# Kernel optimization log

Measured on AMD Instinct MI355X. Metric: run time of the kernel, lower is better.

The kernel has to match this reference:

```python
import jax, jax.numpy as jnp
import numpy as np

N = 50000
E = 800000


def gcn_conv(x, W, b, src, dst, n_nodes):
    # PyG GCNConv: add self-loops, symmetric deg^-1/2 normalization,
    # out[dst] += norm * (x @ W)[src], then bias.
    h = x @ W  # [N, out]
    src_sl = jnp.concatenate([src, jnp.arange(n_nodes, dtype=src.dtype)])
    dst_sl = jnp.concatenate([dst, jnp.arange(n_nodes, dtype=dst.dtype)])
    deg = jax.ops.segment_sum(jnp.ones_like(dst_sl, dtype=h.dtype), dst_sl,
                              num_segments=n_nodes)  # in-degree incl. self-loop
    dinv = jnp.where(deg > 0, jax.lax.rsqrt(deg), 0.0)
    norm = dinv[src_sl] * dinv[dst_sl]  # [E+N]
    msg = norm[:, None] * h[src_sl]  # gather + scale, [E+N, out]
    out = jax.ops.segment_sum(msg, dst_sl, num_segments=n_nodes)
    return out + b


def setup_inputs() -> dict:
    key = jax.random.key(0)
    ks = jax.random.split(key, 8)
    F, H, O = 128, 128, 64
    x = jax.random.normal(ks[0], (N, F), dtype=jnp.float32)
    edge_index = jax.random.randint(ks[1], (2, E), 0, N, dtype=jnp.int64)
    # Glorot-ish scaled weights
    W1 = jax.random.normal(ks[2], (F, H), dtype=jnp.float32) / np.sqrt(F)
    b1 = jnp.zeros((H,), dtype=jnp.float32)
    W2 = jax.random.normal(ks[3], (H, H), dtype=jnp.float32) / np.sqrt(H)
    b2 = jnp.zeros((H,), dtype=jnp.float32)
    W3 = jax.random.normal(ks[4], (H, O), dtype=jnp.float32) / np.sqrt(H)
    b3 = jnp.zeros((O,), dtype=jnp.float32)
    return {"x": x, "edge_index": edge_index, "W1": W1, "b1": b1,
            "W2": W2, "b2": b2, "W3": W3, "b3": b3}


def reference(x, edge_index, W1, b1, W2, b2, W3, b3):
    src, dst = edge_index[0], edge_index[1]
    h = gcn_conv(x, W1, b1, src, dst, N)
    h = jax.nn.elu(h)
    h = gcn_conv(h, W2, b2, src, dst, N)
    h = jax.nn.elu(h)
    h = gcn_conv(h, W3, b3, src, dst, N)
    return h
```

## Files before the change

### kernel.cpp

```cpp
#include <hip/hip_runtime.h>
#include <hip/hip_fp16.h>
#include <math.h>


#define NFEAT_IN 128
#define SCAN_CHUNK 2048

typedef _Float16 f16x8 __attribute__((ext_vector_type(8)));
typedef float f32x4 __attribute__((ext_vector_type(4)));

__global__ void zero_kernel(int4* __restrict__ p, int n4, int4* __restrict__ eswpad) {
    int i = blockIdx.x * blockDim.x + threadIdx.x;
    int4 z; z.x = z.y = z.z = z.w = 0;
    if (i < n4) p[i] = z;
    if (i < 8) eswpad[i] = z;
}

__global__ __launch_bounds__(256) void countrank_kernel(const int* __restrict__ dst,
                                                        int* __restrict__ cnt,
                                                        int* __restrict__ rank, int E) {
    int i = blockIdx.x * blockDim.x + threadIdx.x;
    int base = i * 4;
    if (base + 4 <= E) {
        int4 d = *(const int4*)&dst[base];
        int4 r;
        r.x = atomicAdd(&cnt[d.x], 1);
        r.y = atomicAdd(&cnt[d.y], 1);
        r.z = atomicAdd(&cnt[d.z], 1);
        r.w = atomicAdd(&cnt[d.w], 1);
        *(int4*)&rank[base] = r;
    } else {
        for (int k = base; k < E; ++k) rank[k] = atomicAdd(&cnt[dst[k]], 1);
    }
}

__global__ __launch_bounds__(256) void reduce_kernel(const int* __restrict__ cnt,
                                                     int* __restrict__ bsum, int n) {
    __shared__ int wtot[4];
    int b = blockIdx.x, t = threadIdx.x;
    int base = b * SCAN_CHUNK + t * 8;
    int s = 0;
    if (base + 8 <= n) {
        int4 a = *(const int4*)&cnt[base];
        int4 c = *(const int4*)&cnt[base + 4];
        s = a.x + a.y + a.z + a.w + c.x + c.y + c.z + c.w;
    } else {
        for (int i = 0; i < 8; ++i) if (base + i < n) s += cnt[base + i];
    }
    int lane = t & 63, wid = t >> 6;
    #pragma unroll
    for (int off = 32; off > 0; off >>= 1) s += __shfl_down(s, off, 64);
    if (lane == 0) wtot[wid] = s;
    __syncthreads();
    if (t == 0) bsum[b] = wtot[0] + wtot[1] + wtot[2] + wtot[3];
}

__global__ __launch_bounds__(256) void scan3_kernel(const int* __restrict__ cnt,
                                                    const int* __restrict__ bsum,
                                                    int* __restrict__ offs,
                                                    float* __restrict__ dinv,
                                                    int n, int nb) {
    __shared__ int wtot[4];
    __shared__ int sbase;
    int b = blockIdx.x, t = threadIdx.x;
    if (t < 64) {
        int val = (t < nb) ? bsum[t] : 0;
        int pre = (t < b) ? val : 0;
        int tot = val;
        #pragma unroll
        for (int off = 32; off > 0; off >>= 1) {
            pre += __shfl_down(pre, off, 64);
            tot += __shfl_down(tot, off, 64);
        }
        if (t == 0) {
            sbase = pre;
            if (b == nb - 1) offs[n] = tot;
        }
    }
    int base = b * SCAN_CHUNK + t * 8;
    int v[8];
    #pragma unroll
    for (int i = 0; i < 8; ++i) v[i] = (base + i < n) ? cnt[base + i] : 0;
    int psum[8], s = 0;
    #pragma unroll
    for (int i = 0; i < 8; ++i) { psum[i] = s; s += v[i]; }
    int lane = t & 63, wid = t >> 6;
    int inc = s;
    #pragma unroll
    for (int off = 1; off < 64; off <<= 1) {
        int tt = __shfl_up(inc, off, 64);
        if (lane >= off) inc += tt;
    }
    if (lane == 63) wtot[wid] = inc;
    __syncthreads();
    int wb = 0;
    for (int w = 0; w < wid; ++w) wb += wtot[w];
    int tbase = sbase + wb + (inc - s);
    #pragma unroll
    for (int i = 0; i < 8; ++i) {
        if (base + i < n) {
            offs[base + i] = tbase + psum[i];
            dinv[base + i] = rsqrtf((float)(v[i] + 1));
        }
    }
}

__global__ __launch_bounds__(256) void fillr_kernel(const int* __restrict__ src,
                                                    const int* __restrict__ dst,
                                                    const int* __restrict__ rank,
                                                    const int* __restrict__ offs,
                                                    const float* __restrict__ dinv,
                                                    int2* __restrict__ esw, int E) {
    int i = blockIdx.x * blockDim.x + threadIdx.x;
    int base = i * 4;
    if (base + 4 <= E) {
        int4 d = *(const int4*)&dst[base];
        int4 r = *(const int4*)&rank[base];
        int4 s = *(const int4*)&src[base];
        int p0 = offs[d.x] + r.x;
        int p1 = offs[d.y] + r.y;
        int p2 = offs[d.z] + r.z;
        int p3 = offs[d.w] + r.w;
        float w0 = dinv[s.x], w1 = dinv[s.y], w2 = dinv[s.z], w3 = dinv[s.w];
        __half2 h0 = __floats2half2_rn(w0, w0);
        __half2 h1 = __floats2half2_rn(w1, w1);
        __half2 h2 = __floats2half2_rn(w2, w2);
        __half2 h3 = __floats2half2_rn(w3, w3);
        int2 e0; e0.x = s.x; e0.y = *(int*)&h0;
        int2 e1; e1.x = s.y; e1.y = *(int*)&h1;
        int2 e2; e2.x = s.z; e2.y = *(int*)&h2;
        int2 e3; e3.x = s.w; e3.y = *(int*)&h3;
        esw[p0] = e0; esw[p1] = e1; esw[p2] = e2; esw[p3] = e3;
    } else {
        for (int k = base; k < E; ++k) {
            int d = dst[k];
            int p = offs[d] + rank[k];
            int s = src[k];
            float w = dinv[s];
            __half2 h = __floats2half2_rn(w, w);
            int2 e; e.x = s; e.y = *(int*)&h;
            esw[p] = e;
        }
    }
}

__global__ __launch_bounds__(256) void convx_kernel(const float* __restrict__ x,
                                                    f16x8* __restrict__ Xf, int nchunk) {
    int i = blockIdx.x * blockDim.x + threadIdx.x;
    if (i >= nchunk) return;
    int m = i >> 4, kc = i & 15;
    float4 a = *(const float4*)&x[(size_t)m * 128 + kc * 8];
    float4 b = *(const float4*)&x[(size_t)m * 128 + kc * 8 + 4];
    f16x8 v;
    v[0] = (_Float16)a.x; v[1] = (_Float16)a.y; v[2] = (_Float16)a.z; v[3] = (_Float16)a.w;
    v[4] = (_Float16)b.x; v[5] = (_Float16)b.y; v[6] = (_Float16)b.z; v[7] = (_Float16)b.w;
    int kt = kc >> 2, sub = kc & 3;
    Xf[(size_t)((m >> 4) * 4 + kt) * 64 + sub * 16 + (m & 15)] = v;
}

__global__ void wfrag_kernel(const float* __restrict__ W1, const float* __restrict__ W2,
                             const float* __restrict__ W3, f16x8* __restrict__ wf1,
                             f16x8* __restrict__ wf2, f16x8* __restrict__ wf3) {
    int b = blockIdx.x;
    const float* W; f16x8* Wf; int NT;
    if (b < 8)       { W = W1; Wf = wf1; NT = 8; }
    else if (b < 16) { W = W2; Wf = wf2; NT = 8; b -= 8; }
    else             { W = W3; Wf = wf3; NT = 4; b -= 16; }
    int c = b * 256 + threadIdx.x;
    if (c >= NT * 256) return;
    int BN = NT * 16;
    int nt = c >> 8;
    int kt = (c >> 6) & 3;
    int l = c & 63;
    int n = nt * 16 + (l & 15);
    int k0 = kt * 32 + (l >> 4) * 8;
    f16x8 v;
    #pragma unroll
    for (int j = 0; j < 8; ++j) v[j] = (_Float16)W[(size_t)(k0 + j) * BN + n];
    Wf[c] = v;
}

template <int NT>
__global__ __launch_bounds__(256) void mgemm_kernel(const f16x8* __restrict__ Xf,
                                                    const f16x8* __restrict__ Wg,
                                                    __half* __restrict__ Y, int mtiles) {
    constexpr int BN = NT * 16;
    __shared__ f16x8 Wf[NT * 4 * 64];
    int t = threadIdx.x;
    #pragma unroll
    for (int i = 0; i < NT; ++i) Wf[t + i * 256] = Wg[t + i * 256];
    __syncthreads();
    int lane = t & 63;
    int mt0 = blockIdx.x * 8 + (t >> 6) * 2;
    #pragma unroll
    for (int it = 0; it < 2; ++it) {
        int mtile = mt0 + it;
        if (mtile >= mtiles) continue;
        const f16x8* xb = Xf + (size_t)mtile * 4 * 64;
        f16x8 bf[4];
        #pragma unroll
        for (int kt = 0; kt < 4; ++kt) bf[kt] = xb[kt * 64 + lane];
        f32x4 acc[NT];
        #pragma unroll
        for (int nt = 0; nt < NT; ++nt) acc[nt] = (f32x4){0.f, 0.f, 0.f, 0.f};
        #pragma unroll
        for (int kt = 0; kt < 4; ++kt) {
            #pragma unroll
            for (int nt = 0; nt < NT; ++nt) {
                f16x8 af = Wf[(nt * 4 + kt) * 64 + lane];
                acc[nt] = __builtin_amdgcn_mfma_f32_16x16x32_f16(af, bf[kt], acc[nt], 0, 0, 0);
            }
        }
        int m = mtile * 16 + (lane & 15);
        int nc0 = (lane >> 4) * 4;
        #pragma unroll
        for (int nt = 0; nt < NT; ++nt) {
            union { __half2 h2[2]; uint2 u; } pk;
            pk.h2[0] = __floats2half2_rn(acc[nt][0], acc[nt][1]);
            pk.h2[1] = __floats2half2_rn(acc[nt][2], acc[nt][3]);
            *(uint2*)&Y[(size_t)m * BN + nt * 16 + nc0] = pk.u;
        }
    }
}

__global__ __launch_bounds__(256) void agg128_kernel(const __half* __restrict__ H,
                                                     const int* __restrict__ offs,
                                                     const int2* __restrict__ esw,
                                                     const float* __restrict__ dinv,
                                                     const float* __restrict__ bias,
                                                     uint4* __restrict__ outf, int n) {
    int lane = threadIdx.x & 63;
    int q = lane >> 4;
    int fl = lane & 15;
    int v = blockIdx.x * 4 + (threadIdx.x >> 6);
    if (v >= n) return;
    float dv = dinv[v];
    int e0 = offs[v], e1 = offs[v + 1];
    int cntE = e1 - e0;
    int nfull = cntE >> 4;
    const char* Hb = (const char*)H + fl * 16;
    __half2 acc[4];
    __half2 zh = __floats2half2_rn(0.f, 0.f);
    acc[0] = zh; acc[1] = zh; acc[2] = zh; acc[3] = zh;
    int e = e0 + q;
    for (int i = 0; i < nfull; ++i, e += 16) {
        #pragma unroll
        for (int j = 0; j < 4; ++j) {
            int2 p = esw[e + 4 * j];
            __half2 w2 = *(__half2*)&p.y;
            uint4 hq = *(const uint4*)(Hb + ((size_t)(unsigned)p.x << 8));
            const __half2* h2 = (const __half2*)&hq;
            acc[0] = __hfma2(h2[0], w2, acc[0]);
            acc[1] = __hfma2(h2[1], w2, acc[1]);
            acc[2] = __hfma2(h2[2], w2, acc[2]);
            acc[3] = __hfma2(h2[3], w2, acc[3]);
        }
    }
    if (cntE & 15) {
        #pragma unroll
        for (int j = 0; j < 4; ++j) {
            int ee = e + 4 * j;
            int2 p = esw[ee];
            int wi = (ee < e1) ? p.y : 0;
            __half2 w2 = *(__half2*)&wi;
            uint4 hq = *(const uint4*)(Hb + ((size_t)(unsigned)p.x << 8));
            const __half2* h2 = (const __half2*)&hq;
            acc[0] = __hfma2(h2[0], w2, acc[0]);
            acc[1] = __hfma2(h2[1], w2, acc[1]);
            acc[2] = __hfma2(h2[2], w2, acc[2]);
            acc[3] = __hfma2(h2[3], w2, acc[3]);
        }
    }
    #pragma unroll
    for (int m = 16; m <= 32; m <<= 1) {
        #pragma unroll
        for (int k = 0; k < 4; ++k) {
            int ai = *(int*)&acc[k];
            int bi = __shfl_xor(ai, m, 64);
            acc[k] = __hadd2(acc[k], *(__half2*)&bi);
        }
    }
    if (q == 0) {
        float a[8];
        #pragma unroll
        for (int k = 0; k < 4; ++k) {
            float2 f = __half22float2(acc[k]);
            a[2 * k] = f.x; a[2 * k + 1] = f.y;
        }
        uint4 hq = *(const uint4*)(Hb + ((size_t)(unsigned)v << 8));
        const _Float16* hp = (const _Float16*)&hq;
        float b[8];
        *(float4*)&b[0] = *(const float4*)&bias[fl * 8];
        *(float4*)&b[4] = *(const float4*)&bias[fl * 8 + 4];
        float r[8];
        #pragma unroll
        for (int k = 0; k < 8; ++k) {
            float t2 = fmaf((float)hp[k], dv, a[k]);
            r[k] = fmaf(dv, t2, b[k]);
            r[k] = r[k] > 0.f ? r[k] : (__expf(r[k]) - 1.f);
        }
        union { __half2 h2[4]; uint4 u; } pk;
        pk.h2[0] = __floats2half2_rn(r[0], r[1]);
        pk.h2[1] = __floats2half2_rn(r[2], r[3]);
        pk.h2[2] = __floats2half2_rn(r[4], r[5]);
        pk.h2[3] = __floats2half2_rn(r[6], r[7]);
        int blockc = (v >> 4) * 4 + (fl >> 2);
        int l2 = (fl & 3) * 16 + (v & 15);
        outf[(size_t)blockc * 64 + l2] = pk.u;
    }
}

__global__ __launch_bounds__(256) void agg64_kernel(const __half* __restrict__ H,
                                                    const int* __restrict__ offs,
                                                    const int2* __restrict__ esw,
                                                    const float* __restrict__ dinv,
                                                    const float* __restrict__ bias,
                                                    float* __restrict__ out, int n) {
    int lane = threadIdx.x & 63;
    int q = lane >> 3;
    int fl = lane & 7;
    int v = blockIdx.x * 4 + (threadIdx.x >> 6);
    if (v >= n) return;
    float dv = dinv[v];
    int e0 = offs[v], e1 = offs[v + 1];
    int cntE = e1 - e0;
    int nfull = cntE >> 4;
    const char* Hb = (const char*)H + fl * 16;
    __half2 acc[4];
    __half2 zh = __floats2half2_rn(0.f, 0.f);
    acc[0] = zh; acc[1] = zh; acc[2] = zh; acc[3] = zh;
    int e = e0 + q;
    for (int i = 0; i < nfull; ++i, e += 16) {
        #pragma unroll
        for (int j = 0; j < 2; ++j) {
            int2 p = esw[e + 8 * j];
            __half2 w2 = *(__half2*)&p.y;
            uint4 hq = *(const uint4*)(Hb + ((size_t)(unsigned)p.x << 7));
            const __half2* h2 = (const __half2*)&hq;
            acc[0] = __hfma2(h2[0], w2, acc[0]);
            acc[1] = __hfma2(h2[1], w2, acc[1]);
            acc[2] = __hfma2(h2[2], w2, acc[2]);
            acc[3] = __hfma2(h2[3], w2, acc[3]);
        }
    }
    if (cntE & 15) {
        #pragma unroll
        for (int j = 0; j < 2; ++j) {
            int ee = e + 8 * j;
            int2 p = esw[ee];
            int wi = (ee < e1) ? p.y : 0;
            __half2 w2 = *(__half2*)&wi;
            uint4 hq = *(const uint4*)(Hb + ((size_t)(unsigned)p.x << 7));
            const __half2* h2 = (const __half2*)&hq;
            acc[0] = __hfma2(h2[0], w2, acc[0]);
            acc[1] = __hfma2(h2[1], w2, acc[1]);
            acc[2] = __hfma2(h2[2], w2, acc[2]);
            acc[3] = __hfma2(h2[3], w2, acc[3]);
        }
    }
    #pragma unroll
    for (int m = 8; m <= 32; m <<= 1) {
        #pragma unroll
        for (int k = 0; k < 4; ++k) {
            int ai = *(int*)&acc[k];
            int bi = __shfl_xor(ai, m, 64);
            acc[k] = __hadd2(acc[k], *(__half2*)&bi);
        }
    }
    if (q == 0) {
        float a[8];
        #pragma unroll
        for (int k = 0; k < 4; ++k) {
            float2 f = __half22float2(acc[k]);
            a[2 * k] = f.x; a[2 * k + 1] = f.y;
        }
        uint4 hq = *(const uint4*)(Hb + ((size_t)(unsigned)v << 7));
        const _Float16* hp = (const _Float16*)&hq;
        float b[8];
        *(float4*)&b[0] = *(const float4*)&bias[fl * 8];
        *(float4*)&b[4] = *(const float4*)&bias[fl * 8 + 4];
        float r[8];
        #pragma unroll
        for (int k = 0; k < 8; ++k) {
            float t2 = fmaf((float)hp[k], dv, a[k]);
            r[k] = fmaf(dv, t2, b[k]);
        }
        float4 o0, o1;
        o0.x = r[0]; o0.y = r[1]; o0.z = r[2]; o0.w = r[3];
        o1.x = r[4]; o1.y = r[5]; o1.z = r[6]; o1.w = r[7];
        *(float4*)&out[(size_t)v * 64 + fl * 8] = o0;
        *(float4*)&out[(size_t)v * 64 + fl * 8 + 4] = o1;
    }
}

static inline size_t alignup(size_t x) { return (x + 255) & ~(size_t)255; }

extern "C" void kernel_launch(void* const* d_in, const int* in_sizes, int n_in,
                              void* d_out, int out_size, void* d_ws, size_t ws_size,
                              hipStream_t stream) {
    const float* x  = (const float*)d_in[0];
    const int*   ei = (const int*)d_in[1];
    const float* W1 = (const float*)d_in[2];
    const float* b1 = (const float*)d_in[3];
    const float* W2 = (const float*)d_in[4];
    const float* b2 = (const float*)d_in[5];
    const float* W3 = (const float*)d_in[6];
    const float* b3 = (const float*)d_in[7];
    float* out = (float*)d_out;

    const int N = in_sizes[0] / NFEAT_IN;
    const int E = in_sizes[1] / 2;
    const int* src = ei;
    const int* dst = ei + E;

    char* w = (char*)d_ws;
    int* cnt  = (int*)w;  w += alignup((size_t)N * sizeof(int));
    int* rank = (int*)w;  w += alignup((size_t)E * sizeof(int));
    int* offs = (int*)w;  w += alignup((size_t)(N + 1) * sizeof(int));
    float* dinv = (float*)w; w += alignup((size_t)N * sizeof(float));
    int* bsum = (int*)w;  w += alignup((size_t)64 * sizeof(int));
    int2* esw = (int2*)w; w += alignup((size_t)(E + 16) * sizeof(int2));
    __half* fA = (__half*)w; w += alignup((size_t)N * 128 * sizeof(__half));
    __half* hB = (__half*)w; w += alignup((size_t)N * 128 * sizeof(__half));
    f16x8* wf1 = (f16x8*)w; w += alignup((size_t)2048 * sizeof(f16x8));
    f16x8* wf2 = (f16x8*)w; w += alignup((size_t)2048 * sizeof(f16x8));
    f16x8* wf3 = (f16x8*)w; w += alignup((size_t)1024 * sizeof(f16x8));

    const int nb = (N + SCAN_CHUNK - 1) / SCAN_CHUNK;
    const int mtiles = N / 16;
    const int egrid = (E / 4 + 255) / 256;

    zero_kernel<<<(N / 4 + 255) / 256, 256, 0, stream>>>((int4*)cnt, N / 4, (int4*)(esw + E));
    countrank_kernel<<<egrid, 256, 0, stream>>>(dst, cnt, rank, E);
    reduce_kernel<<<nb, 256, 0, stream>>>(cnt, bsum, N);
    scan3_kernel<<<nb, 256, 0, stream>>>(cnt, bsum, offs, dinv, N, nb);
    fillr_kernel<<<egrid, 256, 0, stream>>>(src, dst, rank, offs, dinv, esw, E);

    wfrag_kernel<<<20, 256, 0, stream>>>(W1, W2, W3, wf1, wf2, wf3);
    convx_kernel<<<(N * 16 + 255) / 256, 256, 0, stream>>>(x, (f16x8*)fA, N * 16);

    int gemm_grid = (mtiles + 7) / 8;
    int agg_grid = (N + 3) / 4;

    mgemm_kernel<8><<<gemm_grid, 256, 0, stream>>>((const f16x8*)fA, wf1, hB, mtiles);
    agg128_kernel<<<agg_grid, 256, 0, stream>>>(hB, offs, esw, dinv, b1, (uint4*)fA, N);
    mgemm_kernel<8><<<gemm_grid, 256, 0, stream>>>((const f16x8*)fA, wf2, hB, mtiles);
    agg128_kernel<<<agg_grid, 256, 0, stream>>>(hB, offs, esw, dinv, b2, (uint4*)fA, N);
    mgemm_kernel<4><<<gemm_grid, 256, 0, stream>>>((const f16x8*)fA, wf3, hB, mtiles);
    agg64_kernel<<<agg_grid, 256, 0, stream>>>(hB, offs, esw, dinv, b3, out, N);
}
```

Baseline: 193.4 us.

## Split 128-wide hidden features into two 64-column planes for aggregation

The GEMM now writes its 128-column fp16 output as two separate N×64 planes. The 128-wide aggregation runs twice as many blocks, each handling one half of the features for a node with 8 lanes per edge row. This shrinks the gathered working set per pass to 128-byte rows, aiming to improve L2/cache hit rates for the random src gathers. The cost is that edge indices and weights are read twice and twice as many blocks are launched.

```diff
diff --git a/kernel.cpp b/kernel.cpp
--- a/kernel.cpp
+++ b/kernel.cpp
@@ -183,8 +183,8 @@
 template <int NT>
 __global__ __launch_bounds__(256) void mgemm_kernel(const f16x8* __restrict__ Xf,
                                                     const f16x8* __restrict__ Wg,
-                                                    __half* __restrict__ Y, int mtiles) {
-    constexpr int BN = NT * 16;
+                                                    __half* __restrict__ Y, int mtiles,
+                                                    size_t hstride) {
     __shared__ f16x8 Wf[NT * 4 * 64];
     int t = threadIdx.x;
     #pragma unroll
@@ -218,37 +218,38 @@
             union { __half2 h2[2]; uint2 u; } pk;
             pk.h2[0] = __floats2half2_rn(acc[nt][0], acc[nt][1]);
             pk.h2[1] = __floats2half2_rn(acc[nt][2], acc[nt][3]);
-            *(uint2*)&Y[(size_t)m * BN + nt * 16 + nc0] = pk.u;
-        }
-    }
-}
-
-__global__ __launch_bounds__(256) void agg128_kernel(const __half* __restrict__ H,
-                                                     const int* __restrict__ offs,
-                                                     const int2* __restrict__ esw,
-                                                     const float* __restrict__ dinv,
-                                                     const float* __restrict__ bias,
-                                                     uint4* __restrict__ outf, int n) {
+            *(uint2*)&Y[(size_t)(nt >> 2) * hstride + (size_t)m * 64 + (nt & 3) * 16 + nc0] = pk.u;
+        }
+    }
+}
+
+__global__ __launch_bounds__(256) void agg128h_kernel(const __half* __restrict__ H,
+                                                      const int* __restrict__ offs,
+                                                      const int2* __restrict__ esw,
+                                                      const float* __restrict__ dinv,
+                                                      const float* __restrict__ bias,
+                                                      uint4* __restrict__ outf, int n) {
+    int half = blockIdx.x & 1;
     int lane = threadIdx.x & 63;
-    int q = lane >> 4;
-    int fl = lane & 15;
-    int v = blockIdx.x * 4 + (threadIdx.x >> 6);
+    int q = lane >> 3;
+    int fl = lane & 7;
+    int v = (blockIdx.x >> 1) * 4 + (threadIdx.x >> 6);
     if (v >= n) return;
     float dv = dinv[v];
     int e0 = offs[v], e1 = offs[v + 1];
     int cntE = e1 - e0;
     int nfull = cntE >> 4;
-    const char* Hb = (const char*)H + fl * 16;
+    const char* Hb = (const char*)H + (size_t)half * n * 128 + fl * 16;
     __half2 acc[4];
     __half2 zh = __floats2half2_rn(0.f, 0.f);
     acc[0] = zh; acc[1] = zh; acc[2] = zh; acc[3] = zh;
     int e = e0 + q;
     for (int i = 0; i < nfull; ++i, e += 16) {
         #pragma unroll
-        for (int j = 0; j < 4; ++j) {
-            int2 p = esw[e + 4 * j];
+        for (int j = 0; j < 2; ++j) {
+            int2 p = esw[e + 8 * j];
             __half2 w2 = *(__half2*)&p.y;
-            uint4 hq = *(const uint4*)(Hb + ((size_t)(unsigned)p.x << 8));
+            uint4 hq = *(const uint4*)(Hb + ((size_t)(unsigned)p.x << 7));
             const __half2* h2 = (const __half2*)&hq;
             acc[0] = __hfma2(h2[0], w2, acc[0]);
             acc[1] = __hfma2(h2[1], w2, acc[1]);
@@ -258,12 +259,12 @@
     }
     if (cntE & 15) {
         #pragma unroll
-        for (int j = 0; j < 4; ++j) {
-            int ee = e + 4 * j;
+        for (int j = 0; j < 2; ++j) {
+            int ee = e + 8 * j;
             int2 p = esw[ee];
             int wi = (ee < e1) ? p.y : 0;
             __half2 w2 = *(__half2*)&wi;
-            uint4 hq = *(const uint4*)(Hb + ((size_t)(unsigned)p.x << 8));
+            uint4 hq = *(const uint4*)(Hb + ((size_t)(unsigned)p.x << 7));
             const __half2* h2 = (const __half2*)&hq;
             acc[0] = __hfma2(h2[0], w2, acc[0]);
             acc[1] = __hfma2(h2[1], w2, acc[1]);
@@ -272,7 +273,7 @@
         }
     }
     #pragma unroll
-    for (int m = 16; m <= 32; m <<= 1) {
+    for (int m = 8; m <= 32; m <<= 1) {
         #pragma unroll
         for (int k = 0; k < 4; ++k) {
             int ai = *(int*)&acc[k];
@@ -287,11 +288,11 @@
             float2 f = __half22float2(acc[k]);
             a[2 * k] = f.x; a[2 * k + 1] = f.y;
         }
-        uint4 hq = *(const uint4*)(Hb + ((size_t)(unsigned)v << 8));
+        uint4 hq = *(const uint4*)(Hb + ((size_t)(unsigned)v << 7));
         const _Float16* hp = (const _Float16*)&hq;
         float b[8];
-        *(float4*)&b[0] = *(const float4*)&bias[fl * 8];
-        *(float4*)&b[4] = *(const float4*)&bias[fl * 8 + 4];
+        *(float4*)&b[0] = *(const float4*)&bias[half * 64 + fl * 8];
+        *(float4*)&b[4] = *(const float4*)&bias[half * 64 + fl * 8 + 4];
         float r[8];
         #pragma unroll
         for (int k = 0; k < 8; ++k) {
@@ -304,8 +305,9 @@
         pk.h2[1] = __floats2half2_rn(r[2], r[3]);
         pk.h2[2] = __floats2half2_rn(r[4], r[5]);
         pk.h2[3] = __floats2half2_rn(r[6], r[7]);
-        int blockc = (v >> 4) * 4 + (fl >> 2);
-        int l2 = (fl & 3) * 16 + (v & 15);
+        int kc = half * 8 + fl;
+        int blockc = (v >> 4) * 4 + (kc >> 2);
+        int l2 = (kc & 3) * 16 + (v & 15);
         outf[(size_t)blockc * 64 + l2] = pk.u;
     }
 }
@@ -429,6 +431,7 @@
     const int nb = (N + SCAN_CHUNK - 1) / SCAN_CHUNK;
     const int mtiles = N / 16;
     const int egrid = (E / 4 + 255) / 256;
+    const size_t hstride = (size_t)N * 64;
 
     zero_kernel<<<(N / 4 + 255) / 256, 256, 0, stream>>>((int4*)cnt, N / 4, (int4*)(esw + E));
     countrank_kernel<<<egrid, 256, 0, stream>>>(dst, cnt, rank, E);
@@ -440,12 +443,13 @@
     convx_kernel<<<(N * 16 + 255) / 256, 256, 0, stream>>>(x, (f16x8*)fA, N * 16);
 
     int gemm_grid = (mtiles + 7) / 8;
-    int agg_grid = (N + 3) / 4;
-
-    mgemm_kernel<8><<<gemm_grid, 256, 0, stream>>>((const f16x8*)fA, wf1, hB, mtiles);
-    agg128_kernel<<<agg_grid, 256, 0, stream>>>(hB, offs, esw, dinv, b1, (uint4*)fA, N);
-    mgemm_kernel<8><<<gemm_grid, 256, 0, stream>>>((const f16x8*)fA, wf2, hB, mtiles);
-    agg128_kernel<<<agg_grid, 256, 0, stream>>>(hB, offs, esw, dinv, b2, (uint4*)fA, N);
-    mgemm_kernel<4><<<gemm_grid, 256, 0, stream>>>((const f16x8*)fA, wf3, hB, mtiles);
-    agg64_kernel<<<agg_grid, 256, 0, stream>>>(hB, offs, esw, dinv, b3, out, N);
-}
+    int agg128_grid = ((N + 3) / 4) * 2;
+    int agg64_grid = (N + 3) / 4;
+
+    mgemm_kernel<8><<<gemm_grid, 256, 0, stream>>>((const f16x8*)fA, wf1, hB, mtiles, hstride);
+    agg128h_kernel<<<agg128_grid, 256, 0, stream>>>(hB, offs, esw, dinv, b1, (uint4*)fA, N);
+    mgemm_kernel<8><<<gemm_grid, 256, 0, stream>>>((const f16x8*)fA, wf2, hB, mtiles, hstride);
+    agg128h_kernel<<<agg128_grid, 256, 0, stream>>>(hB, offs, esw, dinv, b2, (uint4*)fA, N);
+    mgemm_kernel<4><<<gemm_grid, 256, 0, stream>>>((const f16x8*)fA, wf3, hB, mtiles, 0);
+    agg64_kernel<<<agg64_grid, 256, 0, stream>>>(hB, offs, esw, dinv, b3, out, N);
+}
```

Result: slower. 208.6 us (+7.9%).
